# Kernel tuning notes

Measured on AMD Instinct MI355X. Metric: run time of the kernel, lower is better.

The kernel has to match this reference:

```python
import jax, jax.numpy as jnp
import numpy as np

G, N, E = 64, 1000, 8192          # graphs, nodes/graph, edges/graph
F_IN, C, H, HID, NCLS = 128, 128, 4, 256, 2
EPS = 1e-5


def _gcn(x, src, dst, W, b):
    # GCNConv: symmetric normalization with self-loops, sum aggregation.
    h = x @ W                                              # [N, C]
    deg = jax.ops.segment_sum(jnp.ones(E, h.dtype), dst, num_segments=N) + 1.0
    dinv = jax.lax.rsqrt(deg)                              # deg^{-1/2}
    msg = h[src] * (dinv[src] * dinv[dst])[:, None]        # [E, C] gather
    out = jax.ops.segment_sum(msg, dst, num_segments=N)    # scatter-add
    out = out + h * (dinv * dinv)[:, None]                 # self-loop term
    return out + b


def _layernorm(y, g, b):
    mu = y.mean(-1, keepdims=True)
    var = ((y - mu) ** 2).mean(-1, keepdims=True)
    return (y - mu) * jax.lax.rsqrt(var + EPS) * g + b


def setup_inputs() -> dict:
    key = jax.random.key(0)
    ks = jax.random.split(key, 12)
    rn = lambda k, s: jax.random.normal(k, s, jnp.float32) * 0.05
    return dict(
        x=jax.random.normal(ks[0], (G, N, F_IN), jnp.float32),
        edge_index=jax.random.randint(ks[1], (G, 2, E), 0, N),
        W0=rn(ks[2], (F_IN, C)), b0=jnp.zeros((C,), jnp.float32),
        W1=rn(ks[3], (C, C)), b1=jnp.zeros((C,), jnp.float32),
        in_w=rn(ks[4], (3 * C, C)), in_b=jnp.zeros((3 * C,), jnp.float32),
        out_w=rn(ks[5], (C, C)), out_b=jnp.zeros((C,), jnp.float32),
        ln2_g=jnp.ones((C,), jnp.float32), ln2_b=jnp.zeros((C,), jnp.float32),
        mw1=rn(ks[6], (C, HID)), mb1=jnp.zeros((HID,), jnp.float32),
        mw2=rn(ks[7], (HID, C)), mb2=jnp.zeros((C,), jnp.float32),
        lw=rn(ks[8], (C, NCLS)), lb=jnp.zeros((NCLS,), jnp.float32),
    )


def reference(x, edge_index, W0, b0, W1, b1, in_w, in_b, out_w, out_b,
              ln2_g, ln2_b, mw1, mb1, mw2, mb2, lw, lb):
    src, dst = edge_index[:, 0, :], edge_index[:, 1, :]
    conv = jax.vmap(_gcn, in_axes=(0, 0, 0, None, None))
    h = jnp.tanh(conv(x, src, dst, W0, b0))   # [G, N, C]
    h = jnp.tanh(conv(h, src, dst, W1, b1))
    g = h.sum(axis=1)                          # SumAggregation -> [G, C]

    # MultiheadAttention, unbatched: sequence of G graph embeddings
    qkv = g @ in_w.T + in_b
    q, k, v = jnp.split(qkv, 3, axis=-1)
    d = C // H
    qh, kh, vh = (t.reshape(G, H, d) for t in (q, k, v))
    attn = jax.nn.softmax(jnp.einsum('qhd,khd->hqk', qh, kh) * (d ** -0.5), axis=-1)
    o = jnp.einsum('hqk,khd->qhd', attn, vh).reshape(G, C) @ out_w.T + out_b

    x_attend = o                               # dropout = identity (eval)
    # NOTE: original computes layer_norm1(x_attend) but immediately overwrites it.
    mlp = jnp.maximum(x_attend @ mw1 + mb1, 0.0) @ mw2 + mb2
    y = _layernorm(x_attend + mlp, ln2_g, ln2_b)
    node_repr = jnp.maximum(y, 0.0).sum(axis=0)  # [C]
    return node_repr @ lw + lb                   # [NCLS]
```

## Files before the change

kernel.cpp:

```cpp
#include <hip/hip_runtime.h>
#include <math.h>

#define Gn 64
#define Nn 1000
#define En 8192
#define Cc 128
#define HIDn 256
#define EPSf 1e-5f

typedef __attribute__((ext_vector_type(8))) short bh8;
typedef __attribute__((ext_vector_type(4))) float fx4;

__device__ __forceinline__ unsigned short f2bf(float f) {
    unsigned u = __float_as_uint(f);
    u += 0x7fffu + ((u >> 16) & 1u);
    return (unsigned short)(u >> 16);
}
__device__ __forceinline__ float bflo(unsigned u) { return __uint_as_float(u << 16); }
__device__ __forceinline__ float bfhi(unsigned u) { return __uint_as_float(u & 0xffff0000u); }

__global__ __launch_bounds__(256) void k_fused(const int* __restrict__ ei, const float* __restrict__ X,
                                               const float* __restrict__ W, int4* __restrict__ ninfo,
                                               int2* __restrict__ epair, float* __restrict__ pooled,
                                               float* __restrict__ repr, int* __restrict__ ctr,
                                               unsigned short* __restrict__ Hout)
{
    __shared__ __align__(16) short Wt[128][136];
    __shared__ int   curs[1024];
    __shared__ float dinv_s[1024];
    __shared__ int   wsum[4];
    int t = threadIdx.x;

    if (blockIdx.x >= 256) {
        int g = blockIdx.x - 256;
        const int* srcp = ei + (size_t)g * 2 * En;
        const int* dstp = srcp + En;
        int lane = t & 63, wv = t >> 6;

        #pragma unroll
        for (int j = 0; j < 4; ++j) curs[t * 4 + j] = 0;
        __syncthreads();
        for (int e = t; e < En; e += 256) atomicAdd(&curs[dstp[e]], 1);
        __syncthreads();

        int base = t * 4;
        int d0 = curs[base], d1 = curs[base + 1], d2 = curs[base + 2], d3 = curs[base + 3];
        int s = d0 + d1 + d2 + d3;
        int v = s;
        #pragma unroll
        for (int off = 1; off <= 32; off <<= 1) {
            int u = __shfl_up(v, off);
            if (lane >= off) v += u;
        }
        if (lane == 63) wsum[wv] = v;
        __syncthreads();
        int woff = 0;
        #pragma unroll
        for (int w = 0; w < 4; ++w) if (w < wv) woff += wsum[w];
        int e0 = woff + v - s;
        int e1 = e0 + d0, e2 = e1 + d1, e3 = e2 + d2;
        float dv0 = rsqrtf((float)d0 + 1.f), dv1 = rsqrtf((float)d1 + 1.f);
        float dv2 = rsqrtf((float)d2 + 1.f), dv3 = rsqrtf((float)d3 + 1.f);
        curs[base] = e0; curs[base + 1] = e1; curs[base + 2] = e2; curs[base + 3] = e3;
        dinv_s[base] = dv0; dinv_s[base + 1] = dv1; dinv_s[base + 2] = dv2; dinv_s[base + 3] = dv3;
        if (base < Nn)     ninfo[g * Nn + base]     = make_int4(e0, d0, __float_as_int(dv0 * dv0), 0);
        if (base + 1 < Nn) ninfo[g * Nn + base + 1] = make_int4(e1, d1, __float_as_int(dv1 * dv1), 0);
        if (base + 2 < Nn) ninfo[g * Nn + base + 2] = make_int4(e2, d2, __float_as_int(dv2 * dv2), 0);
        if (base + 3 < Nn) ninfo[g * Nn + base + 3] = make_int4(e3, d3, __float_as_int(dv3 * dv3), 0);
        __syncthreads();

        for (int e = t; e < En; e += 256) {
            int dd = dstp[e], ss = srcp[e];
            int p = atomicAdd(&curs[dd], 1);
            float w = dinv_s[ss] * dinv_s[dd];
            epair[(size_t)g * En + p] = make_int2(ss, __float_as_int(w));
        }
        if (t < Cc) pooled[g * Cc + t] = 0.f;
        if (g == 0 && t < Cc) repr[t] = 0.f;
        if (g == 0 && t == 0) *ctr = 0;
        return;
    }

    int b = blockIdx.x;
    int xcd = b & 7, j = b >> 3;
    int g = xcd + 8 * (j & 7);
    int rblk = j >> 3;
    for (int idx = t; idx < 16384; idx += 256) {
        int kI = idx >> 7, n = idx & 127;
        Wt[n][kI] = (short)f2bf(W[idx]);
    }
    __syncthreads();
    int wave = t >> 6, l = t & 63;
    int lr = l & 15, lg = l >> 4;
    const float* Xf = X + (size_t)g * Nn * Cc;
    unsigned short* Hg = Hout + (size_t)g * Nn * Cc;

    for (int s = 0; s < 4; ++s) {
        int rbase = rblk * 256 + wave * 64 + s * 16;
        int r = rbase + lr;
        bool ok = r < Nn;
        bh8 af[4];
        #pragma unroll
        for (int ks = 0; ks < 4; ++ks) {
            if (ok) {
                const float* xp = Xf + (size_t)r * Cc + ks * 32 + lg * 8;
                fx4 a0 = *(const fx4*)xp;
                fx4 a1 = *(const fx4*)(xp + 4);
                bh8 av;
                av[0] = (short)f2bf(a0[0]); av[1] = (short)f2bf(a0[1]);
                av[2] = (short)f2bf(a0[2]); av[3] = (short)f2bf(a0[3]);
                av[4] = (short)f2bf(a1[0]); av[5] = (short)f2bf(a1[1]);
                av[6] = (short)f2bf(a1[2]); av[7] = (short)f2bf(a1[3]);
                af[ks] = av;
            } else af[ks] = bh8{0, 0, 0, 0, 0, 0, 0, 0};
        }
        fx4 acc[8];
        #pragma unroll
        for (int ct = 0; ct < 8; ++ct) acc[ct] = fx4{0.f, 0.f, 0.f, 0.f};
        #pragma unroll
        for (int ks = 0; ks < 4; ++ks) {
            #pragma unroll
            for (int ct = 0; ct < 8; ++ct) {
                bh8 bfr = *(const bh8*)(&Wt[ct * 16 + lr][ks * 32 + lg * 8]);
                acc[ct] = __builtin_amdgcn_mfma_f32_16x16x32_bf16(af[ks], bfr, acc[ct], 0, 0, 0);
            }
        }
        #pragma unroll
        for (int ct = 0; ct < 8; ++ct) {
            #pragma unroll
            for (int rg = 0; rg < 4; ++rg) {
                int row = rbase + lg * 4 + rg;
                if (row < Nn) Hg[(size_t)row * Cc + ct * 16 + lr] = f2bf(acc[ct][rg]);
            }
        }
    }
}

__global__ __launch_bounds__(256) void k_gemm1(const unsigned short* __restrict__ Xh,
                                               const float* __restrict__ W,
                                               unsigned short* __restrict__ Hout)
{
    __shared__ __align__(16) short Wt[128][136];
    int b = blockIdx.x;
    int xcd = b & 7, j = b >> 3;
    int g = xcd + 8 * (j & 7);
    int rblk = j >> 3;
    int t = threadIdx.x;
    for (int idx = t; idx < 16384; idx += 256) {
        int kI = idx >> 7, n = idx & 127;
        Wt[n][kI] = (short)f2bf(W[idx]);
    }
    __syncthreads();
    int wave = t >> 6, l = t & 63;
    int lr = l & 15, lg = l >> 4;
    const short* Xg = (const short*)Xh + (size_t)g * Nn * Cc;
    unsigned short* Hg = Hout + (size_t)g * Nn * Cc;

    for (int s = 0; s < 4; ++s) {
        int rbase = rblk * 256 + wave * 64 + s * 16;
        int r = rbase + lr;
        bool ok = r < Nn;
        bh8 af[4];
        #pragma unroll
        for (int ks = 0; ks < 4; ++ks) {
            if (ok) af[ks] = *(const bh8*)(Xg + (size_t)r * Cc + ks * 32 + lg * 8);
            else    af[ks] = bh8{0, 0, 0, 0, 0, 0, 0, 0};
        }
        fx4 acc[8];
        #pragma unroll
        for (int ct = 0; ct < 8; ++ct) acc[ct] = fx4{0.f, 0.f, 0.f, 0.f};
        #pragma unroll
        for (int ks = 0; ks < 4; ++ks) {
            #pragma unroll
            for (int ct = 0; ct < 8; ++ct) {
                bh8 bfr = *(const bh8*)(&Wt[ct * 16 + lr][ks * 32 + lg * 8]);
                acc[ct] = __builtin_amdgcn_mfma_f32_16x16x32_bf16(af[ks], bfr, acc[ct], 0, 0, 0);
            }
        }
        #pragma unroll
        for (int ct = 0; ct < 8; ++ct) {
            #pragma unroll
            for (int rg = 0; rg < 4; ++rg) {
                int row = rbase + lg * 4 + rg;
                if (row < Nn) Hg[(size_t)row * Cc + ct * 16 + lr] = f2bf(acc[ct][rg]);
            }
        }
    }
}

template<int POOL>
__global__ __launch_bounds__(256) void k_combine(const unsigned* __restrict__ Hb, const int2* __restrict__ epair,
                                                 const int4* __restrict__ ninfo, const float* __restrict__ bias,
                                                 unsigned* __restrict__ Tout, float* __restrict__ pooled)
{
    int b = blockIdx.x;
    int xcd = b & 7, j = b >> 3;
    int g = xcd + 8 * (j & 7);
    int blk = j >> 3;
    int wave = threadIdx.x >> 6, lane = threadIdx.x & 63;
    const unsigned* Hg = Hb + (size_t)g * Nn * 64;
    const int2* epg = epair + (size_t)g * En;
    const int4* nig = ninfo + (size_t)g * Nn;
    float2 bb = *(const float2*)(bias + lane * 2);
    float px = 0.f, py = 0.f;
    for (int n = blk * 4 + wave; n < Nn; n += 128) {
        int4 ni = nig[n];
        int st = ni.x, dc = ni.y;
        float sw = __int_as_float(ni.z);
        unsigned hv = Hg[n * 64 + lane];
        float a0x = bflo(hv) * sw + bb.x, a0y = bfhi(hv) * sw + bb.y;
        float a1x = 0.f, a1y = 0.f, a2x = 0.f, a2y = 0.f, a3x = 0.f, a3y = 0.f;
        int e = 0;
        for (; e + 4 <= dc; e += 4) {
            int2 p0 = epg[st + e];
            int2 p1 = epg[st + e + 1];
            int2 p2 = epg[st + e + 2];
            int2 p3 = epg[st + e + 3];
            unsigned r0 = Hg[p0.x * 64 + lane];
            unsigned r1 = Hg[p1.x * 64 + lane];
            unsigned r2 = Hg[p2.x * 64 + lane];
            unsigned r3 = Hg[p3.x * 64 + lane];
            float w0 = __int_as_float(p0.y), w1 = __int_as_float(p1.y);
            float w2 = __int_as_float(p2.y), w3 = __int_as_float(p3.y);
            a0x = fmaf(bflo(r0), w0, a0x); a0y = fmaf(bfhi(r0), w0, a0y);
            a1x = fmaf(bflo(r1), w1, a1x); a1y = fmaf(bfhi(r1), w1, a1y);
            a2x = fmaf(bflo(r2), w2, a2x); a2y = fmaf(bfhi(r2), w2, a2y);
            a3x = fmaf(bflo(r3), w3, a3x); a3y = fmaf(bfhi(r3), w3, a3y);
        }
        for (; e < dc; ++e) {
            int2 p0 = epg[st + e];
            unsigned r0 = Hg[p0.x * 64 + lane];
            float w0 = __int_as_float(p0.y);
            a0x = fmaf(bflo(r0), w0, a0x); a0y = fmaf(bfhi(r0), w0, a0y);
        }
        float ax = (a0x + a1x) + (a2x + a3x);
        float ay = (a0y + a1y) + (a2y + a3y);
        float tx = tanhf(ax), ty = tanhf(ay);
        if (POOL) { px += tx; py += ty; }
        else Tout[(size_t)(g * Nn + n) * 64 + lane] = ((unsigned)f2bf(ty) << 16) | (unsigned)f2bf(tx);
    }
    if (POOL) {
        atomicAdd(&pooled[g * Cc + lane * 2], px);
        atomicAdd(&pooled[g * Cc + lane * 2 + 1], py);
    }
}

__global__ __launch_bounds__(1024) void k_qkv(const float* __restrict__ pooled, const float* __restrict__ in_w,
                                              const float* __restrict__ in_b, float* __restrict__ qkvb)
{
    int t = threadIdx.x, lane = t & 63, wv = t >> 6;
    int c = blockIdx.x * 16 + wv;
    const float* wr = in_w + c * Cc;
    float w0 = wr[lane], w1 = wr[64 + lane];
    float bias = in_b[c];
    for (int i = 0; i < Gn; ++i) {
        float p = fmaf(pooled[i * Cc + lane], w0, pooled[i * Cc + 64 + lane] * w1);
        #pragma unroll
        for (int off2 = 32; off2 > 0; off2 >>= 1) p += __shfl_xor(p, off2);
        if (lane == 0) qkvb[i * 384 + c] = p + bias;
    }
}

__global__ __launch_bounds__(1024) void k_attn(const float* __restrict__ qkvb, float* __restrict__ ob)
{
    __shared__ float q[64][33], kk[64][33], v[64][33];
    __shared__ float S[64][64];
    int h = blockIdx.x, t = threadIdx.x;

    for (int idx = t; idx < 2048; idx += 1024) {
        int i = idx >> 5, cc = idx & 31;
        q[i][cc]  = qkvb[i * 384 + h * 32 + cc];
        kk[i][cc] = qkvb[i * 384 + 128 + h * 32 + cc];
        v[i][cc]  = qkvb[i * 384 + 256 + h * 32 + cc];
    }
    __syncthreads();

    for (int idx = t; idx < 4096; idx += 1024) {
        int i = idx >> 6, jj = idx & 63;
        float acc = 0.f;
        #pragma unroll
        for (int d2 = 0; d2 < 32; ++d2) acc = fmaf(q[i][d2], kk[jj][d2], acc);
        S[i][jj] = acc * 0.17677669529663687f;
    }
    __syncthreads();

    int lane = t & 63, w = t >> 6;
    for (int r = w; r < 64; r += 16) {
        float val = S[r][lane];
        float m = val;
        #pragma unroll
        for (int off = 32; off > 0; off >>= 1) m = fmaxf(m, __shfl_xor(m, off));
        float e2 = expf(val - m);
        float ssum = e2;
        #pragma unroll
        for (int off = 32; off > 0; off >>= 1) ssum += __shfl_xor(ssum, off);
        S[r][lane] = e2 / ssum;
    }
    __syncthreads();

    for (int idx = t; idx < 2048; idx += 1024) {
        int i = idx >> 5, d2 = idx & 31;
        float acc = 0.f;
        #pragma unroll 4
        for (int k2 = 0; k2 < 64; ++k2) acc = fmaf(S[i][k2], v[k2][d2], acc);
        ob[i * Cc + h * 32 + d2] = acc;
    }
}

__global__ __launch_bounds__(1024) void k_tailfinal(const float* __restrict__ ob, const float* __restrict__ out_w,
                                                    const float* __restrict__ out_b, const float* __restrict__ mw1,
                                                    const float* __restrict__ mb1, const float* __restrict__ mw2,
                                                    const float* __restrict__ mb2, const float* __restrict__ ln2g,
                                                    const float* __restrict__ ln2b, const float* __restrict__ lw,
                                                    const float* __restrict__ lb, float* __restrict__ repr,
                                                    int* __restrict__ ctr, float* __restrict__ out)
{
    __shared__ float sob[4][128];
    __shared__ float sxatt[4][128];
    __shared__ float sm1[4][256];
    __shared__ float spart[4][128];
    __shared__ float pr[128];
    __shared__ int slast;
    int g0 = blockIdx.x * 4;
    int t = threadIdx.x, lane = t & 63, wv = t >> 6;

    if (t < 512) sob[t >> 7][t & 127] = ob[(size_t)(g0 + (t >> 7)) * Cc + (t & 127)];
    if (t < 128) pr[t] = 0.f;
    __syncthreads();

    for (int c = wv; c < Cc; c += 16) {
        float w0 = out_w[c * Cc + lane];
        float w1 = out_w[c * Cc + 64 + lane];
        float bc = out_b[c];
        #pragma unroll
        for (int g = 0; g < 4; ++g) {
            float p = fmaf(sob[g][lane], w0, sob[g][64 + lane] * w1);
            #pragma unroll
            for (int off = 32; off > 0; off >>= 1) p += __shfl_xor(p, off);
            if (lane == 0) sxatt[g][c] = p + bc;
        }
    }
    __syncthreads();

    {
        int j = t & 255, gi = t >> 8;
        float acc = mb1[j];
        #pragma unroll 8
        for (int k = 0; k < Cc; ++k) acc = fmaf(sxatt[gi][k], mw1[k * HIDn + j], acc);
        sm1[gi][j] = fmaxf(acc, 0.f);
    }
    __syncthreads();

    {
        int c = t & 127, gi = (t >> 7) & 3, half = t >> 9;
        int k0 = half * 128;
        float acc = 0.f;
        #pragma unroll 8
        for (int k = 0; k < 128; ++k) acc = fmaf(sm1[gi][k0 + k], mw2[(k0 + k) * Cc + c], acc);
        if (half) spart[gi][c] = acc;
        __syncthreads();
        if (!half) sxatt[gi][c] = sxatt[gi][c] + acc + spart[gi][c] + mb2[c];
    }
    __syncthreads();

    if (t < 256) {
        int g = wv;
        float v0 = sxatt[g][lane], v1 = sxatt[g][64 + lane];
        float s = v0 + v1;
        #pragma unroll
        for (int off = 32; off > 0; off >>= 1) s += __shfl_xor(s, off);
        float mu = s * (1.f / 128.f);
        float d0 = v0 - mu, d1 = v1 - mu;
        float vv = d0 * d0 + d1 * d1;
        #pragma unroll
        for (int off = 32; off > 0; off >>= 1) vv += __shfl_xor(vv, off);
        float rstd = rsqrtf(vv * (1.f / 128.f) + EPSf);
        float z0 = fmaxf(d0 * rstd * ln2g[lane] + ln2b[lane], 0.f);
        float z1 = fmaxf(d1 * rstd * ln2g[64 + lane] + ln2b[64 + lane], 0.f);
        atomicAdd(&pr[lane], z0);
        atomicAdd(&pr[64 + lane], z1);
    }
    __syncthreads();
    if (t < 128) atomicAdd(&repr[t], pr[t]);

    __threadfence();
    __syncthreads();
    if (t == 0) slast = atomicAdd(ctr, 1);
    __syncthreads();
    if (slast == 15) {
        __threadfence();
        __shared__ float r0s[128], r1s[128];
        if (t < 128) {
            float r = __hip_atomic_load(&repr[t], __ATOMIC_RELAXED, __HIP_MEMORY_SCOPE_AGENT);
            r0s[t] = r * lw[t * 2 + 0];
            r1s[t] = r * lw[t * 2 + 1];
        }
        __syncthreads();
        for (int s2 = 64; s2 > 0; s2 >>= 1) {
            if (t < s2) { r0s[t] += r0s[t + s2]; r1s[t] += r1s[t + s2]; }
            __syncthreads();
        }
        if (t == 0) { out[0] = r0s[0] + lb[0]; out[1] = r1s[0] + lb[1]; }
    }
}

extern "C" void kernel_launch(void* const* d_in, const int* in_sizes, int n_in,
                              void* d_out, int out_size, void* d_ws, size_t ws_size,
                              hipStream_t stream)
{
    const float* x     = (const float*)d_in[0];
    const int*   ei    = (const int*)d_in[1];
    const float* W0    = (const float*)d_in[2];
    const float* b0    = (const float*)d_in[3];
    const float* W1    = (const float*)d_in[4];
    const float* b1    = (const float*)d_in[5];
    const float* in_w  = (const float*)d_in[6];
    const float* in_b  = (const float*)d_in[7];
    const float* out_w = (const float*)d_in[8];
    const float* out_b = (const float*)d_in[9];
    const float* ln2g  = (const float*)d_in[10];
    const float* ln2b  = (const float*)d_in[11];
    const float* mw1   = (const float*)d_in[12];
    const float* mb1   = (const float*)d_in[13];
    const float* mw2   = (const float*)d_in[14];
    const float* mb2   = (const float*)d_in[15];
    const float* lw    = (const float*)d_in[16];
    const float* lb    = (const float*)d_in[17];
    float* out = (float*)d_out;
    (void)in_sizes; (void)n_in; (void)out_size; (void)ws_size;

    char* ws = (char*)d_ws;
    size_t off = 0;
    auto carve = [&](size_t bytes) { size_t o = off; off += (bytes + 255) & ~(size_t)255; return o; };
    size_t o_ni    = carve((size_t)Gn * Nn * 16);
    size_t o_ep    = carve((size_t)Gn * En * 8);
    size_t o_pool  = carve((size_t)Gn * Cc * 4);
    size_t o_qkv   = carve((size_t)Gn * 384 * 4);
    size_t o_ob    = carve((size_t)Gn * Cc * 4);
    size_t o_repr  = carve((size_t)Cc * 4);
    size_t o_ctr   = carve(256);
    size_t o_H     = carve((size_t)Gn * Nn * Cc * 2);
    size_t o_T     = carve((size_t)Gn * Nn * Cc * 2);

    int4*  ninfo  = (int4*)(ws + o_ni);
    int2*  epair  = (int2*)(ws + o_ep);
    float* pooled = (float*)(ws + o_pool);
    float* qkvb   = (float*)(ws + o_qkv);
    float* ob     = (float*)(ws + o_ob);
    float* repr   = (float*)(ws + o_repr);
    int*   ctr    = (int*)(ws + o_ctr);
    unsigned short* H = (unsigned short*)(ws + o_H);
    unsigned short* T = (unsigned short*)(ws + o_T);

    k_fused<<<320, 256, 0, stream>>>(ei, x, W0, ninfo, epair, pooled, repr, ctr, H);
    k_combine<0><<<2048, 256, 0, stream>>>((const unsigned*)H, epair, ninfo, b0, (unsigned*)T, nullptr);
    k_gemm1<<<256, 256, 0, stream>>>(T, W1, H);
    k_combine<1><<<2048, 256, 0, stream>>>((const unsigned*)H, epair, ninfo, b1, nullptr, pooled);
    k_qkv<<<24, 1024, 0, stream>>>(pooled, in_w, in_b, qkvb);
    k_attn<<<4, 1024, 0, stream>>>(qkvb, ob);
    k_tailfinal<<<16, 1024, 0, stream>>>(ob, out_w, out_b, mw1, mb1, mw2, mb2, ln2g, ln2b,
                                         lw, lb, repr, ctr, out);
}
```

Before: 171.9 us.

## Split preprocessing from GEMM, pre-convert weights once, use smaller GEMM blocks

Moves the CSR build and the bf16 weight transpose into a separate pre-kernel, which writes transposed bf16 W0 and W1 to workspace once. The GEMMs become a single templated kernel with one 16-row tile per wave and four times as many blocks (1024), loading pre-converted weights with vector copies instead of converting fp32 per block. This is meant to remove redundant per-block weight conversion and raise parallelism. In exchange it adds a kernel launch and serializes the GEMM0 work after the CSR build, where the old fused kernel overlapped them.

```diff
diff --git a/kernel.cpp b/kernel.cpp
--- a/kernel.cpp
+++ b/kernel.cpp
@@ -19,87 +19,118 @@
 __device__ __forceinline__ float bflo(unsigned u) { return __uint_as_float(u << 16); }
 __device__ __forceinline__ float bfhi(unsigned u) { return __uint_as_float(u & 0xffff0000u); }
 
-__global__ __launch_bounds__(256) void k_fused(const int* __restrict__ ei, const float* __restrict__ X,
-                                               const float* __restrict__ W, int4* __restrict__ ninfo,
-                                               int2* __restrict__ epair, float* __restrict__ pooled,
-                                               float* __restrict__ repr, int* __restrict__ ctr,
-                                               unsigned short* __restrict__ Hout)
-{
-    __shared__ __align__(16) short Wt[128][136];
+__global__ __launch_bounds__(256) void k_pre(const int* __restrict__ ei,
+                                             const float* __restrict__ W0, const float* __restrict__ W1,
+                                             int4* __restrict__ ninfo, int2* __restrict__ epair,
+                                             float* __restrict__ pooled, float* __restrict__ repr,
+                                             int* __restrict__ ctr,
+                                             unsigned short* __restrict__ Wt0g,
+                                             unsigned short* __restrict__ Wt1g)
+{
     __shared__ int   curs[1024];
     __shared__ float dinv_s[1024];
     __shared__ int   wsum[4];
+    __shared__ __align__(16) short Wls[128][136];
     int t = threadIdx.x;
 
-    if (blockIdx.x >= 256) {
-        int g = blockIdx.x - 256;
-        const int* srcp = ei + (size_t)g * 2 * En;
-        const int* dstp = srcp + En;
-        int lane = t & 63, wv = t >> 6;
-
-        #pragma unroll
-        for (int j = 0; j < 4; ++j) curs[t * 4 + j] = 0;
+    if (blockIdx.x >= 64) {
+        const float* Wsrc = (blockIdx.x == 64) ? W0 : W1;
+        unsigned short* Wdst = (blockIdx.x == 64) ? Wt0g : Wt1g;
+        for (int idx = t; idx < 16384; idx += 256) {
+            int kI = idx >> 7, n = idx & 127;
+            Wls[n][kI] = (short)f2bf(Wsrc[idx]);
+        }
         __syncthreads();
-        for (int e = t; e < En; e += 256) atomicAdd(&curs[dstp[e]], 1);
-        __syncthreads();
-
-        int base = t * 4;
-        int d0 = curs[base], d1 = curs[base + 1], d2 = curs[base + 2], d3 = curs[base + 3];
-        int s = d0 + d1 + d2 + d3;
-        int v = s;
-        #pragma unroll
-        for (int off = 1; off <= 32; off <<= 1) {
-            int u = __shfl_up(v, off);
-            if (lane >= off) v += u;
-        }
-        if (lane == 63) wsum[wv] = v;
-        __syncthreads();
-        int woff = 0;
-        #pragma unroll
-        for (int w = 0; w < 4; ++w) if (w < wv) woff += wsum[w];
-        int e0 = woff + v - s;
-        int e1 = e0 + d0, e2 = e1 + d1, e3 = e2 + d2;
-        float dv0 = rsqrtf((float)d0 + 1.f), dv1 = rsqrtf((float)d1 + 1.f);
-        float dv2 = rsqrtf((float)d2 + 1.f), dv3 = rsqrtf((float)d3 + 1.f);
-        curs[base] = e0; curs[base + 1] = e1; curs[base + 2] = e2; curs[base + 3] = e3;
-        dinv_s[base] = dv0; dinv_s[base + 1] = dv1; dinv_s[base + 2] = dv2; dinv_s[base + 3] = dv3;
-        if (base < Nn)     ninfo[g * Nn + base]     = make_int4(e0, d0, __float_as_int(dv0 * dv0), 0);
-        if (base + 1 < Nn) ninfo[g * Nn + base + 1] = make_int4(e1, d1, __float_as_int(dv1 * dv1), 0);
-        if (base + 2 < Nn) ninfo[g * Nn + base + 2] = make_int4(e2, d2, __float_as_int(dv2 * dv2), 0);
-        if (base + 3 < Nn) ninfo[g * Nn + base + 3] = make_int4(e3, d3, __float_as_int(dv3 * dv3), 0);
-        __syncthreads();
-
-        for (int e = t; e < En; e += 256) {
-            int dd = dstp[e], ss = srcp[e];
-            int p = atomicAdd(&curs[dd], 1);
-            float w = dinv_s[ss] * dinv_s[dd];
-            epair[(size_t)g * En + p] = make_int2(ss, __float_as_int(w));
-        }
-        if (t < Cc) pooled[g * Cc + t] = 0.f;
-        if (g == 0 && t < Cc) repr[t] = 0.f;
-        if (g == 0 && t == 0) *ctr = 0;
+        for (int idx = t; idx < 2048; idx += 256) {
+            int n = idx >> 4, kc = idx & 15;
+            bh8 v = *(const bh8*)&Wls[n][kc * 8];
+            *(bh8*)(Wdst + (size_t)idx * 8) = v;
+        }
         return;
     }
 
+    int g = blockIdx.x;
+    const int* srcp = ei + (size_t)g * 2 * En;
+    const int* dstp = srcp + En;
+    int lane = t & 63, wv = t >> 6;
+
+    #pragma unroll
+    for (int j = 0; j < 4; ++j) curs[t * 4 + j] = 0;
+    __syncthreads();
+    for (int e = t; e < En; e += 256) atomicAdd(&curs[dstp[e]], 1);
+    __syncthreads();
+
+    int base = t * 4;
+    int d0 = curs[base], d1 = curs[base + 1], d2 = curs[base + 2], d3 = curs[base + 3];
+    int s = d0 + d1 + d2 + d3;
+    int v = s;
+    #pragma unroll
+    for (int off = 1; off <= 32; off <<= 1) {
+        int u = __shfl_up(v, off);
+        if (lane >= off) v += u;
+    }
+    if (lane == 63) wsum[wv] = v;
+    __syncthreads();
+    int woff = 0;
+    #pragma unroll
+    for (int w = 0; w < 4; ++w) if (w < wv) woff += wsum[w];
+    int e0 = woff + v - s;
+    int e1 = e0 + d0, e2 = e1 + d1, e3 = e2 + d2;
+    float dv0 = rsqrtf((float)d0 + 1.f), dv1 = rsqrtf((float)d1 + 1.f);
+    float dv2 = rsqrtf((float)d2 + 1.f), dv3 = rsqrtf((float)d3 + 1.f);
+    curs[base] = e0; curs[base + 1] = e1; curs[base + 2] = e2; curs[base + 3] = e3;
+    dinv_s[base] = dv0; dinv_s[base + 1] = dv1; dinv_s[base + 2] = dv2; dinv_s[base + 3] = dv3;
+    if (base < Nn)     ninfo[g * Nn + base]     = make_int4(e0, d0, __float_as_int(dv0 * dv0), 0);
+    if (base + 1 < Nn) ninfo[g * Nn + base + 1] = make_int4(e1, d1, __float_as_int(dv1 * dv1), 0);
+    if (base + 2 < Nn) ninfo[g * Nn + base + 2] = make_int4(e2, d2, __float_as_int(dv2 * dv2), 0);
+    if (base + 3 < Nn) ninfo[g * Nn + base + 3] = make_int4(e3, d3, __float_as_int(dv3 * dv3), 0);
+    __syncthreads();
+
+    for (int e = t; e < En; e += 256) {
+        int dd = dstp[e], ss = srcp[e];
+        int p = atomicAdd(&curs[dd], 1);
+        float w = dinv_s[ss] * dinv_s[dd];
+        epair[(size_t)g * En + p] = make_int2(ss, __float_as_int(w));
+    }
+    if (t < Cc) pooled[g * Cc + t] = 0.f;
+    if (g == 0 && t < Cc) repr[t] = 0.f;
+    if (g == 0 && t == 0) *ctr = 0;
+}
+
+template<int INBF>
+__global__ __launch_bounds__(256) void k_gemm(const void* __restrict__ Xin,
+                                              const unsigned short* __restrict__ Wtg,
+                                              unsigned short* __restrict__ Hout)
+{
+    __shared__ __align__(16) short Wt[128][136];
     int b = blockIdx.x;
-    int xcd = b & 7, j = b >> 3;
-    int g = xcd + 8 * (j & 7);
-    int rblk = j >> 3;
-    for (int idx = t; idx < 16384; idx += 256) {
-        int kI = idx >> 7, n = idx & 127;
-        Wt[n][kI] = (short)f2bf(W[idx]);
-    }
-    __syncthreads();
+    int xcd = b & 7, gg = (b >> 3) & 7, rblk = b >> 6;
+    int g = xcd + 8 * gg;
+    int t = threadIdx.x;
+    for (int idx = t; idx < 2048; idx += 256) {
+        int n = idx >> 4, kc = idx & 15;
+        bh8 v = *(const bh8*)(Wtg + (size_t)idx * 8);
+        *(bh8*)&Wt[n][kc * 8] = v;
+    }
+    __syncthreads();
+
     int wave = t >> 6, l = t & 63;
     int lr = l & 15, lg = l >> 4;
-    const float* Xf = X + (size_t)g * Nn * Cc;
+    const float* Xf = (const float*)Xin + (size_t)g * Nn * Cc;
+    const short* Xh = (const short*)Xin + (size_t)g * Nn * Cc;
     unsigned short* Hg = Hout + (size_t)g * Nn * Cc;
 
-    for (int s = 0; s < 4; ++s) {
-        int rbase = rblk * 256 + wave * 64 + s * 16;
-        int r = rbase + lr;
-        bool ok = r < Nn;
-        bh8 af[4];
+    int rbase = rblk * 64 + wave * 16;
+    int r = rbase + lr;
+    bool ok = r < Nn;
+    bh8 af[4];
+    if (INBF) {
+        #pragma unroll
+        for (int ks = 0; ks < 4; ++ks) {
+            if (ok) af[ks] = *(const bh8*)(Xh + (size_t)r * Cc + ks * 32 + lg * 8);
+            else    af[ks] = bh8{0, 0, 0, 0, 0, 0, 0, 0};
+        }
+    } else {
         #pragma unroll
         for (int ks = 0; ks < 4; ++ks) {
             if (ok) {
@@ -114,76 +145,24 @@
                 af[ks] = av;
             } else af[ks] = bh8{0, 0, 0, 0, 0, 0, 0, 0};
         }
-        fx4 acc[8];
-        #pragma unroll
-        for (int ct = 0; ct < 8; ++ct) acc[ct] = fx4{0.f, 0.f, 0.f, 0.f};
-        #pragma unroll
-        for (int ks = 0; ks < 4; ++ks) {
-            #pragma unroll
-            for (int ct = 0; ct < 8; ++ct) {
-                bh8 bfr = *(const bh8*)(&Wt[ct * 16 + lr][ks * 32 + lg * 8]);
-                acc[ct] = __builtin_amdgcn_mfma_f32_16x16x32_bf16(af[ks], bfr, acc[ct], 0, 0, 0);
-            }
-        }
+    }
+    fx4 acc[8];
+    #pragma unroll
+    for (int ct = 0; ct < 8; ++ct) acc[ct] = fx4{0.f, 0.f, 0.f, 0.f};
+    #pragma unroll
+    for (int ks = 0; ks < 4; ++ks) {
         #pragma unroll
         for (int ct = 0; ct < 8; ++ct) {
-            #pragma unroll
-            for (int rg = 0; rg < 4; ++rg) {
-                int row = rbase + lg * 4 + rg;
-                if (row < Nn) Hg[(size_t)row * Cc + ct * 16 + lr] = f2bf(acc[ct][rg]);
-            }
-        }
-    }
-}
-
-__global__ __launch_bounds__(256) void k_gemm1(const unsigned short* __restrict__ Xh,
-                                               const float* __restrict__ W,
-                                               unsigned short* __restrict__ Hout)
-{
-    __shared__ __align__(16) short Wt[128][136];
-    int b = blockIdx.x;
-    int xcd = b & 7, j = b >> 3;
-    int g = xcd + 8 * (j & 7);
-    int rblk = j >> 3;
-    int t = threadIdx.x;
-    for (int idx = t; idx < 16384; idx += 256) {
-        int kI = idx >> 7, n = idx & 127;
-        Wt[n][kI] = (short)f2bf(W[idx]);
-    }
-    __syncthreads();
-    int wave = t >> 6, l = t & 63;
-    int lr = l & 15, lg = l >> 4;
-    const short* Xg = (const short*)Xh + (size_t)g * Nn * Cc;
-    unsigned short* Hg = Hout + (size_t)g * Nn * Cc;
-
-    for (int s = 0; s < 4; ++s) {
-        int rbase = rblk * 256 + wave * 64 + s * 16;
-        int r = rbase + lr;
-        bool ok = r < Nn;
-        bh8 af[4];
-        #pragma unroll
-        for (int ks = 0; ks < 4; ++ks) {
-            if (ok) af[ks] = *(const bh8*)(Xg + (size_t)r * Cc + ks * 32 + lg * 8);
-            else    af[ks] = bh8{0, 0, 0, 0, 0, 0, 0, 0};
-        }
-        fx4 acc[8];
-        #pragma unroll
-        for (int ct = 0; ct < 8; ++ct) acc[ct] = fx4{0.f, 0.f, 0.f, 0.f};
-        #pragma unroll
-        for (int ks = 0; ks < 4; ++ks) {
-            #pragma unroll
-            for (int ct = 0; ct < 8; ++ct) {
-                bh8 bfr = *(const bh8*)(&Wt[ct * 16 + lr][ks * 32 + lg * 8]);
-                acc[ct] = __builtin_amdgcn_mfma_f32_16x16x32_bf16(af[ks], bfr, acc[ct], 0, 0, 0);
-            }
-        }
-        #pragma unroll
-        for (int ct = 0; ct < 8; ++ct) {
-            #pragma unroll
-            for (int rg = 0; rg < 4; ++rg) {
-                int row = rbase + lg * 4 + rg;
-                if (row < Nn) Hg[(size_t)row * Cc + ct * 16 + lr] = f2bf(acc[ct][rg]);
-            }
+            bh8 bfr = *(const bh8*)(&Wt[ct * 16 + lr][ks * 32 + lg * 8]);
+            acc[ct] = __builtin_amdgcn_mfma_f32_16x16x32_bf16(af[ks], bfr, acc[ct], 0, 0, 0);
+        }
+    }
+    #pragma unroll
+    for (int ct = 0; ct < 8; ++ct) {
+        #pragma unroll
+        for (int rg = 0; rg < 4; ++rg) {
+            int row = rbase + lg * 4 + rg;
+            if (row < Nn) Hg[(size_t)row * Cc + ct * 16 + lr] = f2bf(acc[ct][rg]);
         }
     }
 }
@@ -216,10 +195,10 @@
             int2 p1 = epg[st + e + 1];
             int2 p2 = epg[st + e + 2];
             int2 p3 = epg[st + e + 3];
-            unsigned r0 = Hg[p0.x * 64 + lane];
-            unsigned r1 = Hg[p1.x * 64 + lane];
-            unsigned r2 = Hg[p2.x * 64 + lane];
-            unsigned r3 = Hg[p3.x * 64 + lane];
+            unsigned r0 = Hg[(size_t)p0.x * 64 + lane];
+            unsigned r1 = Hg[(size_t)p1.x * 64 + lane];
+            unsigned r2 = Hg[(size_t)p2.x * 64 + lane];
+            unsigned r3 = Hg[(size_t)p3.x * 64 + lane];
             float w0 = __int_as_float(p0.y), w1 = __int_as_float(p1.y);
             float w2 = __int_as_float(p2.y), w3 = __int_as_float(p3.y);
             a0x = fmaf(bflo(r0), w0, a0x); a0y = fmaf(bfhi(r0), w0, a0y);
@@ -229,7 +208,7 @@
         }
         for (; e < dc; ++e) {
             int2 p0 = epg[st + e];
-            unsigned r0 = Hg[p0.x * 64 + lane];
+            unsigned r0 = Hg[(size_t)p0.x * 64 + lane];
             float w0 = __int_as_float(p0.y);
             a0x = fmaf(bflo(r0), w0, a0x); a0y = fmaf(bfhi(r0), w0, a0y);
         }
@@ -439,6 +418,8 @@
     size_t o_ob    = carve((size_t)Gn * Cc * 4);
     size_t o_repr  = carve((size_t)Cc * 4);
     size_t o_ctr   = carve(256);
+    size_t o_W0t   = carve((size_t)Cc * Cc * 2);
+    size_t o_W1t   = carve((size_t)Cc * Cc * 2);
     size_t o_H     = carve((size_t)Gn * Nn * Cc * 2);
     size_t o_T     = carve((size_t)Gn * Nn * Cc * 2);
 
@@ -449,12 +430,15 @@
     float* ob     = (float*)(ws + o_ob);
     float* repr   = (float*)(ws + o_repr);
     int*   ctr    = (int*)(ws + o_ctr);
-    unsigned short* H = (unsigned short*)(ws + o_H);
-    unsigned short* T = (unsigned short*)(ws + o_T);
-
-    k_fused<<<320, 256, 0, stream>>>(ei, x, W0, ninfo, epair, pooled, repr, ctr, H);
+    unsigned short* Wt0g = (unsigned short*)(ws + o_W0t);
+    unsigned short* Wt1g = (unsigned short*)(ws + o_W1t);
+    unsigned short* H  = (unsigned short*)(ws + o_H);
+    unsigned short* T  = (unsigned short*)(ws + o_T);
+
+    k_pre<<<66, 256, 0, stream>>>(ei, W0, W1, ninfo, epair, pooled, repr, ctr, Wt0g, Wt1g);
+    k_gemm<0><<<1024, 256, 0, stream>>>(x, Wt0g, H);
     k_combine<0><<<2048, 256, 0, stream>>>((const unsigned*)H, epair, ninfo, b0, (unsigned*)T, nullptr);
-    k_gemm1<<<256, 256, 0, stream>>>(T, W1, H);
+    k_gemm<1><<<1024, 256, 0, stream>>>(T, Wt1g, H);
     k_combine<1><<<2048, 256, 0, stream>>>((const unsigned*)H, epair, ninfo, b1, nullptr, pooled);
     k_qkv<<<24, 1024, 0, stream>>>(pooled, in_w, in_b, qkvb);
     k_attn<<<4, 1024, 0, stream>>>(qkvb, ob);
```

Result: slower. 178.3 us (+3.7%).
